# Optimization experiments

Hardware: AMD Instinct MI355X
Metric: run time of the kernel (lower is better)

Reference implementation:

```python
import jax, jax.numpy as jnp
import numpy as np

B, NK = 32, 1024
NUM_SAMPLES = 512
IT_MATCHES = 4
IT_RANSAC = 8
NUM_CORR = 5
INLIER_3D_TH = 0.15
INLIER_REF_TH = 0.15
NUM_REF_STEPS = 4
SCORE_TEMP = 10.0
TH_OUTLIERS = 0.35
MAX_LOSS_NULL = 0.5
SOFT_CLIP_M = 0.5
BETA = 5.0 / INLIER_3D_TH


def _gumbel(key, shape):
    u = jax.random.uniform(key, shape, minval=1e-6, maxval=1.0 - 1e-6)
    return -jnp.log(-jnp.log(u))


def _backproject(cor, d, K):
    # cor [B,S,2], d [B,S,2] (channel 0 is depth), K [B,3,3] -> [B,S,3]
    depth = d[..., :1]
    pts = jnp.concatenate([cor, jnp.ones_like(cor[..., :1])], -1)
    Kinv = jnp.linalg.inv(K)
    rays = jnp.einsum('bij,bsj->bsi', Kinv, pts)
    return depth * rays


def _procrustes(X, Y, w):
    # weighted Kabsch: find R,t with Y ~ R X + t. X,Y [B,N,3], w [B,N]
    wn = w / (jnp.sum(w, -1, keepdims=True) + 1e-8)
    muX = jnp.einsum('bn,bni->bi', wn, X)
    muY = jnp.einsum('bn,bni->bi', wn, Y)
    Xc = X - muX[:, None]
    Yc = Y - muY[:, None]
    H = jnp.einsum('bn,bni,bnj->bij', wn, Xc, Yc)  # [B,3,3]
    U, S, Vt = jnp.linalg.svd(H, full_matrices=False)
    V = jnp.swapaxes(Vt, -1, -2)
    Ut = jnp.swapaxes(U, -1, -2)
    d = jnp.linalg.det(V @ Ut)
    Vm = V * jnp.stack([jnp.ones_like(d), jnp.ones_like(d), d], -1)[:, None, :]
    R = Vm @ Ut
    t = muY - jnp.einsum('bij,bj->bi', R, muX)
    return R, t[:, None, :]


def _dist(X, Y, R, t):
    return jnp.linalg.norm(jnp.einsum('bij,bnj->bni', R, X) + t - Y, axis=-1)


def _pose_loss(R, t, Rgt, tgt):
    cosang = jnp.clip((jnp.einsum('bij,bij->b', R, Rgt) - 1.0) / 2.0, -0.999999, 0.999999)
    ang = jnp.arccos(cosang)
    terr = jnp.linalg.norm(t - tgt, axis=-1)[:, 0]
    sc = lambda x: SOFT_CLIP_M * jnp.tanh(x / SOFT_CLIP_M)
    lr = sc(ang)[:, None]
    lt = sc(terr)[:, None]
    return 0.5 * (lr + lt), lr, lt


def _rodrigues(axis, ang):
    x, y, z = axis[:, 0], axis[:, 1], axis[:, 2]
    zero = jnp.zeros_like(x)
    Kx = jnp.stack([zero, -z, y, z, zero, -x, -y, x, zero], -1).reshape(-1, 3, 3)
    I = jnp.eye(3, dtype=axis.dtype)[None]
    return I + jnp.sin(ang)[:, None, None] * Kx + (1.0 - jnp.cos(ang))[:, None, None] * (Kx @ Kx)


def setup_inputs():
    ks = jax.random.split(jax.random.key(0), 10)
    matches = jax.random.uniform(ks[0], (B, NK, NK), jnp.float32, 1e-4, 1.0)
    kps0 = jax.random.uniform(ks[1], (B, 2, NK), jnp.float32, 0.0, 640.0)
    kps1 = jax.random.uniform(ks[2], (B, 2, NK), jnp.float32, 0.0, 640.0)
    depth0 = jax.random.uniform(ks[3], (B, 2, NK), jnp.float32, 0.1, 10.0)
    depth1 = jax.random.uniform(ks[4], (B, 2, NK), jnp.float32, 0.1, 10.0)
    Kc = jnp.tile(jnp.array([[600.0, 0.0, 320.0], [0.0, 600.0, 240.0], [0.0, 0.0, 1.0]], jnp.float32)[None], (B, 1, 1))
    axis = jax.random.normal(ks[5], (B, 3))
    axis = axis / (jnp.linalg.norm(axis, axis=-1, keepdims=True) + 1e-8)
    ang = jax.random.uniform(ks[6], (B,), minval=0.0, maxval=0.5)
    R = _rodrigues(axis, ang)
    tvec = 0.3 * jax.random.normal(ks[7], (B, 3))
    T = jnp.zeros((B, 4, 4), jnp.float32).at[:, :3, :3].set(R).at[:, :3, 3].set(tvec).at[:, 3, 3].set(1.0)
    return dict(matches=matches, kps0=kps0, depth0=depth0, kps1=kps1, depth1=depth1,
                K0=Kc, K1=Kc, Kori_color0=Kc, T_0to1=T)


def _forward(matches, kps0, depth0, kps1, depth1, K0, K1, T_0to1):
    Rgt = T_0to1[:, :3, :3]
    tgt = T_0to1[:, :3, 3][:, None, :]
    matches_row = matches.reshape(B, NK * NK)
    logm = jnp.log(matches_row + 1e-12)
    bidx = jnp.arange(B)[:, None]
    kps0t = jnp.swapaxes(kps0, 1, 2)  # [B,NK,2]
    kps1t = jnp.swapaxes(kps1, 1, 2)
    d0t = jnp.swapaxes(depth0, 1, 2)
    d1t = jnp.swapaxes(depth1, 1, 2)
    key = jax.random.key(42)
    total = jnp.zeros((B, 1), jnp.float32)
    for _i in range(IT_MATCHES):
        key, km = jax.random.split(key)
        # multinomial-without-replacement via Gumbel top-k over the full match matrix
        _, sidx = jax.lax.top_k(logm + _gumbel(km, logm.shape), NUM_SAMPLES)  # [B,S]
        i0 = sidx // NK
        i1 = sidx % NK
        cor0 = kps0t[bidx, i0]
        cor1 = kps1t[bidx, i1]
        dd0 = d0t[bidx, i0]
        dd1 = d1t[bidx, i1]
        w = matches_row[bidx, sidx]  # sampling weights for RANSAC minimal sets
        X = _backproject(cor0, dd0, K0)
        Y = _backproject(cor1, dd1, K1)
        logw = jnp.log(w + 1e-12)
        scores, lvals = [], []
        for _kk in range(IT_RANSAC):
            key, kr = jax.random.split(key)
            _, ridx = jax.lax.top_k(logw + _gumbel(kr, logw.shape), NUM_CORR)  # [B,C]
            Xk = X[bidx, ridx]
            Yk = Y[bidx, ridx]
            R_pre, t_pre = _procrustes(Xk, Yk, jnp.ones((B, NUM_CORR), X.dtype))  # use_weights=False
            score_k = jnp.sum(jax.nn.sigmoid(BETA * (INLIER_3D_TH - _dist(X, Y, R_pre, t_pre))), -1, keepdims=True)
            # inlier refinement (no_grad in original)
            Xd = jax.lax.stop_gradient(X)
            Yd = jax.lax.stop_gradient(Y)
            Rd = jax.lax.stop_gradient(R_pre)
            td = jax.lax.stop_gradient(t_pre)
            inl_ref = jnp.zeros((B, NUM_SAMPLES), X.dtype).at[bidx, ridx].set(1.0)
            inl_pre = jnp.zeros((B,), X.dtype)
            for _r in range(NUM_REF_STEPS):
                inl = (_dist(Xd, Yd, Rd, td) < INLIER_REF_TH).astype(X.dtype)
                cnt = inl.sum(-1)
                do = (cnt >= NUM_CORR) & (cnt > inl_pre)
                inl_pre = cnt
                inl_ref = jnp.where(do[:, None], inl, inl_ref)
                Rn, tn = _procrustes(Xd, Yd, inl_ref)
                Rd = jnp.where(do[:, None, None], Rn, Rd)
                td = jnp.where(do[:, None, None], tn, td)
            R, t = _procrustes(X, Y, inl_ref)  # differentiable final fit
            lv, _lr, _lt = _pose_loss(R, t, Rgt, tgt)
            scores.append(score_k)
            lvals.append(lv)
        scores_r = jnp.concatenate(scores, -1)  # [B,IT_RANSAC]
        lvals_r = jnp.concatenate(lvals, -1)
        null_score = TH_OUTLIERS * NUM_SAMPLES * jnp.ones((B, 1), jnp.float32)
        null_loss = MAX_LOSS_NULL * jnp.ones((B, 1), jnp.float32)
        scores_n = jnp.concatenate([scores_r, null_score], -1)
        lvals_n = jnp.concatenate([lvals_r, null_loss], -1)
        sm = jax.nn.softmax(scores_n / SCORE_TEMP, -1)
        total = total + jnp.sum(lvals_n * sm, -1, keepdims=True)
    return total / IT_MATCHES


def reference(matches, kps0, depth0, kps1, depth1, K0, K1, Kori_color0, T_0to1):
    return _forward(matches, kps0, depth0, kps1, depth1, K0, K1, T_0to1)
```

## Files before the change

### kernel.cpp

```cpp
#include <hip/hip_runtime.h>
#include <stdint.h>

typedef unsigned long long u64;
typedef uint32_t u32;

#define NB 32
#define NKP 1024
#define ROWN (NKP*NKP)
#define NSAMP 512
#define ITM 4
#define ITR 8
#define NBIN 2048
#define KBASE 0xC0000000u
#define CHUNKS 64
#define SLOTS 256
#define QCAP 768

struct Keys { u32 km[ITM][2]; u32 kr[ITM][ITR][2]; };

__host__ __device__ static inline u32 rotl32(u32 x, int d) { return __builtin_rotateleft32(x, (unsigned)d); }

__host__ __device__ static inline void tf2x32(u32 k0, u32 k1, u32 x0, u32 x1, u32& o0, u32& o1)
{
    u32 ks2 = k0 ^ k1 ^ 0x1BD11BDAu;
    x0 += k0; x1 += k1;
#define TFR(r) { x0 += x1; x1 = rotl32(x1, r); x1 ^= x0; }
    TFR(13) TFR(15) TFR(26) TFR(6)
    x0 += k1; x1 += ks2 + 1u;
    TFR(17) TFR(29) TFR(16) TFR(24)
    x0 += ks2; x1 += k0 + 2u;
    TFR(13) TFR(15) TFR(26) TFR(6)
    x0 += k0; x1 += k1 + 3u;
    TFR(17) TFR(29) TFR(16) TFR(24)
    x0 += k1; x1 += ks2 + 4u;
    TFR(13) TFR(15) TFR(26) TFR(6)
    x0 += ks2; x1 += k0 + 5u;
#undef TFR
    o0 = x0; o1 = x1;
}

#define G_MINV 1e-6f
#define G_MAXV ((float)(1.0 - 1e-6))
#define G_SPAN (G_MAXV - G_MINV)

__device__ static inline float u_from_bits(u32 bits) {
    float f = __uint_as_float((bits >> 9) | 0x3f800000u) - 1.0f;
    float u = __fadd_rn(__fmul_rn(f, G_SPAN), G_MINV);
    return fmaxf(G_MINV, u);
}

#define EARLY_TH9 (8220000u << 9)

__device__ static inline u32 fkey(float v) {
    u32 u = __float_as_uint(v);
    return (u & 0x80000000u) ? ~u : (u | 0x80000000u);
}

__device__ static inline float wred(float v) {
    #pragma unroll
    for (int o = 1; o < 64; o <<= 1) v += __shfl_xor(v, o, 64);
    return v;
}

__device__ static inline u64 shfl_xor_u64(u64 v, int mask) {
    u32 lo = (u32)v, hi = (u32)(v >> 32);
    lo = __shfl_xor(lo, mask, 64);
    hi = __shfl_xor(hi, mask, 64);
    return ((u64)hi << 32) | (u64)lo;
}

__device__ static void kabsch(const float Hf[9], float Rf[9])
{
    double H00=Hf[0],H01=Hf[1],H02=Hf[2];
    double H10=Hf[3],H11=Hf[4],H12=Hf[5];
    double H20=Hf[6],H21=Hf[7],H22=Hf[8];
    double A00 = H00*H00 + H10*H10 + H20*H20;
    double A01 = H00*H01 + H10*H11 + H20*H21;
    double A02 = H00*H02 + H10*H12 + H20*H22;
    double A11 = H01*H01 + H11*H11 + H21*H21;
    double A12 = H01*H02 + H11*H12 + H21*H22;
    double A22 = H02*H02 + H12*H12 + H22*H22;
    double V00=1,V10=0,V20=0;
    double V01=0,V11=1,V21=0;
    double V02=0,V12=0,V22=1;
#define JROT(App,Aqq,Apq,Apr,Aqr, Vp0,Vp1,Vp2, Vq0,Vq1,Vq2) \
    if (fabs(Apq) > 0.0) { \
        double th = (Aqq - App) / (2.0 * Apq); \
        double tt = copysign(1.0, th) / (fabs(th) + sqrt(1.0 + th*th)); \
        double cc = 1.0 / sqrt(1.0 + tt*tt); \
        double ss = tt * cc; \
        double npp = App - tt*Apq, nqq = Aqq + tt*Apq; \
        double npr = cc*Apr - ss*Aqr, nqr = ss*Apr + cc*Aqr; \
        App = npp; Aqq = nqq; Apq = 0.0; Apr = npr; Aqr = nqr; \
        double tv; \
        tv = cc*Vp0 - ss*Vq0; Vq0 = ss*Vp0 + cc*Vq0; Vp0 = tv; \
        tv = cc*Vp1 - ss*Vq1; Vq1 = ss*Vp1 + cc*Vq1; Vp1 = tv; \
        tv = cc*Vp2 - ss*Vq2; Vq2 = ss*Vp2 + cc*Vq2; Vp2 = tv; \
    }
    for (int sw = 0; sw < 10; ++sw) {
        JROT(A00,A11,A01, A02,A12, V00,V10,V20, V01,V11,V21);
        JROT(A00,A22,A02, A01,A12, V00,V10,V20, V02,V12,V22);
        JROT(A11,A22,A12, A01,A02, V01,V11,V21, V02,V12,V22);
    }
#undef JROT
    double l0=A00, l1=A11, l2=A22;
    double e0[3]={V00,V10,V20}, e1[3]={V01,V11,V21}, e2[3]={V02,V12,V22};
    if (l0 < l1) { double t=l0;l0=l1;l1=t; for(int c=0;c<3;++c){double s=e0[c];e0[c]=e1[c];e1[c]=s;} }
    if (l0 < l2) { double t=l0;l0=l2;l2=t; for(int c=0;c<3;++c){double s=e0[c];e0[c]=e2[c];e2[c]=s;} }
    if (l1 < l2) { double t=l1;l1=l2;l2=t; for(int c=0;c<3;++c){double s=e1[c];e1[c]=e2[c];e2[c]=s;} }
    double u0[3], u1[3], u2[3];
#define HMUL(e,u) { u[0]=H00*e[0]+H01*e[1]+H02*e[2]; u[1]=H10*e[0]+H11*e[1]+H12*e[2]; u[2]=H20*e[0]+H21*e[1]+H22*e[2]; }
    HMUL(e0,u0) HMUL(e1,u1) HMUL(e2,u2)
#undef HMUL
    double s0 = sqrt(u0[0]*u0[0]+u0[1]*u0[1]+u0[2]*u0[2]);
    double s1 = sqrt(u1[0]*u1[0]+u1[1]*u1[1]+u1[2]*u1[2]);
    double s2 = sqrt(u2[0]*u2[0]+u2[1]*u2[1]+u2[2]*u2[2]);
    double eps = 1e-12 + 1e-6 * s0;
    if (s0 > 0.0) { u0[0]/=s0; u0[1]/=s0; u0[2]/=s0; } else { u0[0]=1.0; u0[1]=0.0; u0[2]=0.0; }
    if (s1 > eps) { u1[0]/=s1; u1[1]/=s1; u1[2]/=s1; }
    else {
        double ax0 = (fabs(u0[0]) < 0.9) ? 1.0 : 0.0;
        double ax1 = 1.0 - ax0;
        double dd = ax0*u0[0] + ax1*u0[1];
        double w0 = ax0 - dd*u0[0], w1 = ax1 - dd*u0[1], w2 = -dd*u0[2];
        double nn = sqrt(w0*w0+w1*w1+w2*w2);
        u1[0]=w0/nn; u1[1]=w1/nn; u1[2]=w2/nn;
    }
    if (s2 > eps) { u2[0]/=s2; u2[1]/=s2; u2[2]/=s2; }
    else {
        u2[0] = u0[1]*u1[2] - u0[2]*u1[1];
        u2[1] = u0[2]*u1[0] - u0[0]*u1[2];
        u2[2] = u0[0]*u1[1] - u0[1]*u1[0];
    }
    double M[3][3];
    #pragma unroll
    for (int i2=0;i2<3;++i2)
      #pragma unroll
      for (int j2=0;j2<3;++j2)
        M[i2][j2] = e0[i2]*u0[j2] + e1[i2]*u1[j2] + e2[i2]*u2[j2];
    double det = M[0][0]*(M[1][1]*M[2][2]-M[1][2]*M[2][1])
               - M[0][1]*(M[1][0]*M[2][2]-M[1][2]*M[2][0])
               + M[0][2]*(M[1][0]*M[2][1]-M[1][1]*M[2][0]);
    #pragma unroll
    for (int i2=0;i2<3;++i2)
      #pragma unroll
      for (int j2=0;j2<3;++j2)
        Rf[i2*3+j2] = (float)(e0[i2]*u0[j2] + e1[i2]*u1[j2] + det*(e2[i2]*u2[j2]));
}

__device__ static inline float dist1(const float R[9], const float t[3], const float x[3], const float y[3])
{
    float a = R[0]*x[0]+R[1]*x[1]+R[2]*x[2]+t[0]-y[0];
    float b = R[3]*x[0]+R[4]*x[1]+R[5]*x[2]+t[1]-y[1];
    float c = R[6]*x[0]+R[7]*x[1]+R[8]*x[2]+t[2]-y[2];
    return sqrtf(a*a+b*b+c*c);
}

__device__ static void proc512(const float (&X)[8][3], const float (&Y)[8][3], const float (&w)[8],
                               float R[9], float t[3])
{
    float sw = 0.f;
    #pragma unroll
    for (int q=0;q<8;++q) sw += w[q];
    float S = wred(sw) + 1e-8f;
    float wn[8];
    #pragma unroll
    for (int q=0;q<8;++q) wn[q] = w[q] / S;
    float mx[3], my[3];
    #pragma unroll
    for (int c=0;c<3;++c) {
        float ax=0.f, ay=0.f;
        #pragma unroll
        for (int q=0;q<8;++q) { ax += wn[q]*X[q][c]; ay += wn[q]*Y[q][c]; }
        mx[c] = wred(ax); my[c] = wred(ay);
    }
    float Hf[9];
    #pragma unroll
    for (int ci=0;ci<3;++ci)
      #pragma unroll
      for (int cj=0;cj<3;++cj) {
        float h=0.f;
        #pragma unroll
        for (int q=0;q<8;++q) h += wn[q]*(X[q][ci]-mx[ci])*(Y[q][cj]-my[cj]);
        Hf[ci*3+cj] = wred(h);
      }
    kabsch(Hf, R);
    #pragma unroll
    for (int c=0;c<3;++c) t[c] = my[c] - (R[c*3+0]*mx[0] + R[c*3+1]*mx[1] + R[c*3+2]*mx[2]);
}

__device__ static void inv3(const float* __restrict__ Kin, float* __restrict__ out)
{
    float a[3][6];
    for (int r=0;r<3;++r) for (int c=0;c<3;++c) { a[r][c]=Kin[r*3+c]; a[r][c+3] = (r==c)?1.f:0.f; }
    for (int col=0; col<3; ++col) {
        int piv = col;
        for (int r=col+1;r<3;++r) if (fabsf(a[r][col]) > fabsf(a[piv][col])) piv = r;
        if (piv != col) for (int c=0;c<6;++c) { float tt=a[col][c]; a[col][c]=a[piv][c]; a[piv][c]=tt; }
        float pv = a[col][col];
        for (int c=0;c<6;++c) a[col][c] /= pv;
        for (int r=0;r<3;++r) if (r != col) {
            float f = a[r][col];
            if (f != 0.f) for (int c=0;c<6;++c) a[r][c] -= f * a[col][c];
        }
    }
    for (int r=0;r<3;++r) for (int c=0;c<3;++c) out[r*3+c] = a[r][c+3];
}

static const size_t OFF_CNTS = 0;
static const size_t OFF_SC   = OFF_CNTS + (size_t)ITM*NB*CHUNKS*4;
static const size_t OFF_LV   = OFF_SC   + (size_t)ITM*NB*ITR*4;
static const size_t OFF_SAMP = OFF_LV   + (size_t)ITM*NB*ITR*4;
static const size_t OFF_CAND = OFF_SAMP + (size_t)ITM*NB*NSAMP*8*4;

__global__ __launch_bounds__(256) void kA(const float* __restrict__ mat, Keys keys,
                                          u64* __restrict__ candC, u32* __restrict__ cnts)
{
    __shared__ u64 lists[ITM][SLOTS];
    __shared__ u32 lcnt[ITM];
    __shared__ u32 qbits[QCAP];
    __shared__ float qm[QCAP];
    __shared__ u32 qji[QCAP];
    __shared__ u32 qcnt;
    int tid = threadIdx.x;
    int b = blockIdx.y;
    int chunk = blockIdx.x;
    if (tid < ITM) lcnt[tid] = 0;
    if (tid == 0) qcnt = 0;
    __syncthreads();
    const float4* rowp = reinterpret_cast<const float4*>(mat + (size_t)b * ROWN);
    int base = chunk * 4096;
    for (int itc = 0; itc < 16; ++itc) {
        int f4 = base + itc*256 + tid;
        float4 m4 = rowp[f4];
        float mv[4] = {m4.x, m4.y, m4.z, m4.w};
        u32 j0 = (u32)f4 * 4u;
        #pragma unroll
        for (int e = 0; e < 4; ++e) {
            u32 j = j0 + (u32)e;
            u32 flat = ((u32)b << 20) | j;
            #pragma unroll
            for (int i = 0; i < ITM; ++i) {
                u32 o0, o1; tf2x32(keys.km[i][0], keys.km[i][1], 0u, flat, o0, o1);
                u32 bits = o0 ^ o1;
                if (bits >= EARLY_TH9) {
                    u32 p = atomicAdd(&qcnt, 1u);
                    if (p < (u32)QCAP) {
                        qbits[p] = bits;
                        qm[p]    = mv[e];
                        qji[p]   = ((u32)i << 20) | j;
                    }
                }
            }
        }
        __syncthreads();
        u32 qn = qcnt; if (qn > (u32)QCAP) qn = QCAP;
        for (u32 t = tid; t < qn; t += 256) {
            u32 bits = qbits[t];
            float m  = qm[t];
            u32 ji   = qji[t];
            float u  = u_from_bits(bits);
            float g  = -logf(-logf(u));
            float lg = logf(m + 1e-12f);
            float v  = lg + g;
            if (v > 4.0f) {
                u32 i2 = ji >> 20;
                u32 jj = ji & 0xFFFFFu;
                u32 p = atomicAdd(&lcnt[i2], 1u);
                if (p < (u32)SLOTS)
                    lists[i2][p] = ((u64)fkey(v) << 32) | (u64)(u32)(~jj);
            }
        }
        __syncthreads();
        if (tid == 0) qcnt = 0;
        __syncthreads();
    }
    #pragma unroll
    for (int i = 0; i < ITM; ++i) {
        u32 n = lcnt[i]; if (n > (u32)SLOTS) n = SLOTS;
        for (u32 s = tid; s < n; s += 256)
            candC[(((size_t)(i*NB + b))*CHUNKS + chunk)*SLOTS + s] = lists[i][s];
    }
    if (tid < ITM) cnts[((size_t)(tid*NB + b))*CHUNKS + chunk] = min(lcnt[tid], (u32)SLOTS);
}

__global__ __launch_bounds__(256) void kD(const float* __restrict__ mat,
        const float* __restrict__ kps0, const float* __restrict__ dep0,
        const float* __restrict__ kps1, const float* __restrict__ dep1,
        const float* __restrict__ K0, const float* __restrict__ K1,
        const u64* __restrict__ candC, const u32* __restrict__ cnts,
        float* __restrict__ samp)
{
    int ib = blockIdx.x;
    int b = ib % NB;
    int tid = threadIdx.x;
    __shared__ u32 hist[NBIN];
    __shared__ u64 buf[2048];
    __shared__ u32 ccnt[CHUNKS];
    __shared__ u32 gs[64];
    __shared__ u32 nkeep, cutkey_s;
    __shared__ float Ki[2][9];
    for (int idx = tid; idx < NBIN; idx += 256) hist[idx] = 0;
    for (int idx = tid; idx < 2048; idx += 256) buf[idx] = 0ull;
    if (tid < CHUNKS) ccnt[tid] = cnts[(size_t)ib*CHUNKS + tid];
    if (tid == 0) nkeep = 0;
    __syncthreads();
    const u64* cd = candC + (size_t)ib * CHUNKS * SLOTS;
    for (int t = tid; t < CHUNKS*SLOTS; t += 256) {
        int c = t >> 8, s = t & (SLOTS-1);
        if ((u32)s < ccnt[c]) {
            u32 key = (u32)(cd[t] >> 32);
            u32 bin = (key - KBASE) >> 14;
            if (bin > (u32)(NBIN-1)) bin = NBIN-1;
            atomicAdd(&hist[bin], 1u);
        }
    }
    __syncthreads();
    if (tid < 64) {
        u32 ssum = 0;
        int top = NBIN-1 - tid*32;
        for (int k = 0; k < 32; ++k) ssum += hist[top - k];
        gs[tid] = ssum;
    }
    __syncthreads();
    if (tid == 0) {
        u32 cum = 0; int cutbin = -1;
        for (int g = 0; g < 64; ++g) {
            if (cum + gs[g] >= (u32)NSAMP) {
                int t2 = NBIN-1 - g*32;
                for (int k = 0; k < 32; ++k) {
                    u32 c = hist[t2 - k];
                    if (cum + c >= (u32)NSAMP) { cutbin = t2 - k; break; }
                    cum += c;
                }
                break;
            }
            cum += gs[g];
        }
        cutkey_s = (cutbin >= 0) ? (KBASE + ((u32)cutbin << 14)) : 0u;
    }
    __syncthreads();
    u32 cutkey = cutkey_s;
    for (int t = tid; t < CHUNKS*SLOTS; t += 256) {
        int c = t >> 8, s = t & (SLOTS-1);
        if ((u32)s < ccnt[c]) {
            u64 cv = cd[t];
            if ((u32)(cv >> 32) >= cutkey) {
                u32 p = atomicAdd(&nkeep, 1u);
                if (p < 2048u) buf[p] = cv;
            }
        }
    }
    __syncthreads();
    for (int k = 2; k <= 2048; k <<= 1) {
        for (int j = k >> 1; j > 0; j >>= 1) {
            for (int i2 = tid; i2 < 2048; i2 += 256) {
                int ixj = i2 ^ j;
                if (ixj > i2) {
                    bool up = ((i2 & k) == 0);
                    u64 a = buf[i2], c2 = buf[ixj];
                    bool dosw = up ? (a > c2) : (a < c2);
                    if (dosw) { buf[i2] = c2; buf[ixj] = a; }
                }
            }
            __syncthreads();
        }
    }
    if (tid == 0) { inv3(K0 + (size_t)b*9, Ki[0]); inv3(K1 + (size_t)b*9, Ki[1]); }
    __syncthreads();
    for (int r = tid; r < NSAMP; r += 256) {
        u64 c = buf[2047 - r];
        u32 j = (~(u32)(c & 0xFFFFFFFFull)) & (u32)(ROWN - 1);
        int i0 = (int)(j >> 10);
        int i1 = (int)(j & 1023u);
        float uu0 = kps0[(size_t)b*2*NKP + i0];
        float vv0 = kps0[(size_t)b*2*NKP + NKP + i0];
        float dd0 = dep0[(size_t)b*2*NKP + i0];
        float uu1 = kps1[(size_t)b*2*NKP + i1];
        float vv1 = kps1[(size_t)b*2*NKP + NKP + i1];
        float dd1 = dep1[(size_t)b*2*NKP + i1];
        float r0 = Ki[0][0]*uu0 + Ki[0][1]*vv0 + Ki[0][2];
        float r1 = Ki[0][3]*uu0 + Ki[0][4]*vv0 + Ki[0][5];
        float r2 = Ki[0][6]*uu0 + Ki[0][7]*vv0 + Ki[0][8];
        float q0 = Ki[1][0]*uu1 + Ki[1][1]*vv1 + Ki[1][2];
        float q1 = Ki[1][3]*uu1 + Ki[1][4]*vv1 + Ki[1][5];
        float q2 = Ki[1][6]*uu1 + Ki[1][7]*vv1 + Ki[1][8];
        float w = mat[(size_t)b*ROWN + j];
        float* sp = samp + ((size_t)ib*NSAMP + r)*8;
        sp[0] = dd0*r0; sp[1] = dd0*r1; sp[2] = dd0*r2;
        sp[3] = dd1*q0; sp[4] = dd1*q1; sp[5] = dd1*q2;
        sp[6] = logf(w + 1e-12f);
        sp[7] = 0.f;
    }
}

__global__ __launch_bounds__(64) void kE(const float* __restrict__ samp, const float* __restrict__ Tmat,
                                         Keys keys, float* __restrict__ scoreArr, float* __restrict__ lvArr)
{
    int blk = blockIdx.x;
    int kk = blk & 7;
    int ib = blk >> 3;
    int i = ib / NB;
    int b = ib % NB;
    int lane = threadIdx.x;
    const float* s = samp + (size_t)ib * NSAMP * 8;
    float X[8][3], Y[8][3], lw[8];
    #pragma unroll
    for (int q = 0; q < 8; ++q) {
        const float4* p = reinterpret_cast<const float4*>(s + (size_t)(q*64 + lane)*8);
        float4 a0 = p[0], a1 = p[1];
        X[q][0]=a0.x; X[q][1]=a0.y; X[q][2]=a0.z;
        Y[q][0]=a0.w; Y[q][1]=a1.x; Y[q][2]=a1.y;
        lw[q]=a1.z;
    }
    u64 comp[8];
    #pragma unroll
    for (int q = 0; q < 8; ++q) {
        u32 j = (u32)(q*64 + lane);
        u32 o0,o1; tf2x32(keys.kr[i][kk][0], keys.kr[i][kk][1], 0u, (u32)(b*NSAMP) + j, o0,o1);
        float u = u_from_bits(o0^o1);
        float g = -logf(-logf(u));
        float v = lw[q] + g;
        comp[q] = ((u64)fkey(v) << 32) | (u64)(u32)(~j);
    }
    int ridx[5];
    #pragma unroll
    for (int r = 0; r < 5; ++r) {
        u64 m = comp[0];
        #pragma unroll
        for (int q=1;q<8;++q) if (comp[q] > m) m = comp[q];
        #pragma unroll
        for (int o=1;o<64;o<<=1) { u64 x = shfl_xor_u64(m,o); if (x > m) m = x; }
        ridx[r] = (int)((~(u32)(m & 0xFFFFFFFFull)) & (u32)(NSAMP-1));
        #pragma unroll
        for (int q=0;q<8;++q) if (comp[q] == m) comp[q] = 0ull;
    }
    float Xk[5][3], Yk[5][3];
    #pragma unroll
    for (int r=0;r<5;++r) {
        const float* p = s + (size_t)ridx[r]*8;
        Xk[r][0]=p[0]; Xk[r][1]=p[1]; Xk[r][2]=p[2];
        Yk[r][0]=p[3]; Yk[r][1]=p[4]; Yk[r][2]=p[5];
    }
    float S5 = 5.0f + 1e-8f;
    float wn5 = 1.0f / S5;
    float mx[3]={0,0,0}, my[3]={0,0,0};
    #pragma unroll
    for (int r=0;r<5;++r) {
        #pragma unroll
        for (int c=0;c<3;++c) { mx[c] += wn5*Xk[r][c]; my[c] += wn5*Yk[r][c]; }
    }
    float Hf[9] = {0,0,0,0,0,0,0,0,0};
    #pragma unroll
    for (int r=0;r<5;++r)
      #pragma unroll
      for (int ci=0;ci<3;++ci)
        #pragma unroll
        for (int cj=0;cj<3;++cj)
          Hf[ci*3+cj] += wn5*(Xk[r][ci]-mx[ci])*(Yk[r][cj]-my[cj]);
    float Rpre[9], tpre[3];
    kabsch(Hf, Rpre);
    #pragma unroll
    for (int c=0;c<3;++c) tpre[c] = my[c] - (Rpre[c*3+0]*mx[0] + Rpre[c*3+1]*mx[1] + Rpre[c*3+2]*mx[2]);
    const float BETAF = (float)(5.0/0.15);
    float partial = 0.f;
    #pragma unroll
    for (int q=0;q<8;++q) {
        float d = dist1(Rpre, tpre, X[q], Y[q]);
        float z = BETAF * (0.15f - d);
        partial += 1.0f / (1.0f + expf(-z));
    }
    float score = wred(partial);
    float inlref[8];
    #pragma unroll
    for (int q=0;q<8;++q) {
        int j = q*64 + lane;
        inlref[q] = (j==ridx[0] || j==ridx[1] || j==ridx[2] || j==ridx[3] || j==ridx[4]) ? 1.0f : 0.0f;
    }
    float Rd[9], td[3];
    #pragma unroll
    for (int c2=0;c2<9;++c2) Rd[c2]=Rpre[c2];
    td[0]=tpre[0]; td[1]=tpre[1]; td[2]=tpre[2];
    float inl_pre = 0.f;
    for (int step=0; step<4; ++step) {
        float inl[8]; float csum = 0.f;
        #pragma unroll
        for (int q=0;q<8;++q) {
            float d = dist1(Rd, td, X[q], Y[q]);
            inl[q] = (d < 0.15f) ? 1.0f : 0.0f;
            csum += inl[q];
        }
        float cnt = wred(csum);
        bool doit = (cnt >= 5.0f) && (cnt > inl_pre);
        inl_pre = cnt;
        if (doit) {
            #pragma unroll
            for (int q=0;q<8;++q) inlref[q] = inl[q];
            proc512(X, Y, inlref, Rd, td);
        }
    }
    float Rfin[9], tfin[3];
    proc512(X, Y, inlref, Rfin, tfin);
    const float* Tb = Tmat + (size_t)b*16;
    float tr = 0.f;
    #pragma unroll
    for (int ci=0;ci<3;++ci)
      #pragma unroll
      for (int cj=0;cj<3;++cj)
        tr += Rfin[ci*3+cj] * Tb[ci*4+cj];
    float cosang = (tr - 1.0f) * 0.5f;
    cosang = fminf(fmaxf(cosang, -0.999999f), 0.999999f);
    float ang = acosf(cosang);
    float d0 = tfin[0]-Tb[3], d1 = tfin[1]-Tb[7], d2 = tfin[2]-Tb[11];
    float terr = sqrtf(d0*d0 + d1*d1 + d2*d2);
    float lr = 0.5f * tanhf(ang / 0.5f);
    float lt = 0.5f * tanhf(terr / 0.5f);
    float lv = 0.5f * (lr + lt);
    if (lane == 0) { scoreArr[blk] = score; lvArr[blk] = lv; }
}

__global__ void kF(const float* __restrict__ scoreArr, const float* __restrict__ lvArr, float* __restrict__ out)
{
    int b = threadIdx.x;
    if (b >= NB) return;
    const float NULLSC = (float)(0.35 * 512.0);
    float total = 0.f;
    for (int i = 0; i < ITM; ++i) {
        float x[9], lvv[9], ee[9];
        for (int k = 0; k < 8; ++k) {
            x[k] = scoreArr[(i*NB + b)*ITR + k] / 10.0f;
            lvv[k] = lvArr[(i*NB + b)*ITR + k];
        }
        x[8] = NULLSC / 10.0f;
        lvv[8] = 0.5f;
        float m = x[0];
        for (int k = 1; k < 9; ++k) m = fmaxf(m, x[k]);
        float Ssum = 0.f;
        for (int k = 0; k < 9; ++k) { ee[k] = expf(x[k] - m); Ssum += ee[k]; }
        float acc = 0.f;
        for (int k = 0; k < 9; ++k) acc += lvv[k] * (ee[k] / Ssum);
        total += acc;
    }
    out[b] = total / 4.0f;
}

extern "C" void kernel_launch(void* const* d_in, const int* in_sizes, int n_in,
                              void* d_out, int out_size, void* d_ws, size_t ws_size,
                              hipStream_t stream)
{
    (void)in_sizes; (void)n_in; (void)out_size; (void)ws_size;
    const float* mat  = (const float*)d_in[0];
    const float* kps0 = (const float*)d_in[1];
    const float* dep0 = (const float*)d_in[2];
    const float* kps1 = (const float*)d_in[3];
    const float* dep1 = (const float*)d_in[4];
    const float* K0   = (const float*)d_in[5];
    const float* K1   = (const float*)d_in[6];
    const float* Tm   = (const float*)d_in[8];
    float* out = (float*)d_out;

    Keys keys;
    {
        u32 k0 = 0u, k1 = 42u;
        for (int i = 0; i < ITM; ++i) {
            u32 a0,a1,b0,b1;
            tf2x32(k0,k1, 0u,0u, a0,a1);
            tf2x32(k0,k1, 0u,1u, b0,b1);
            k0=a0; k1=a1; keys.km[i][0]=b0; keys.km[i][1]=b1;
            for (int kk = 0; kk < ITR; ++kk) {
                tf2x32(k0,k1, 0u,0u, a0,a1);
                tf2x32(k0,k1, 0u,1u, b0,b1);
                k0=a0; k1=a1; keys.kr[i][kk][0]=b0; keys.kr[i][kk][1]=b1;
            }
        }
    }
    char* ws = (char*)d_ws;
    u32* cnts       = (u32*)(ws + OFF_CNTS);
    float* scoreArr = (float*)(ws + OFF_SC);
    float* lvArr    = (float*)(ws + OFF_LV);
    float* samp     = (float*)(ws + OFF_SAMP);
    u64* candC      = (u64*)(ws + OFF_CAND);

    kA<<<dim3(CHUNKS, NB), 256, 0, stream>>>(mat, keys, candC, cnts);
    kD<<<ITM*NB, 256, 0, stream>>>(mat, kps0, dep0, kps1, dep1, K0, K1, candC, cnts, samp);
    kE<<<ITM*NB*ITR, 64, 0, stream>>>(samp, Tm, keys, scoreArr, lvArr);
    kF<<<1, 64, 0, stream>>>(scoreArr, lvArr, out);
}
```

Before: 406.8 us.

## Gather match values only for queued candidates instead of streaming full matrix

The candidate pass no longer streams every match value through float4 loads. It hashes indices only, packs bits, iteration and index into a single 64-bit shared queue entry, and loads the match value from global memory just for the queued candidates. Queue flushes drop from 16 to 4 per chunk, so there are fewer block barriers, and the queue capacity grows to fit the larger batches. The trade-off is scattered global gathers, and a higher risk of the queue overflowing and silently dropping candidates.

```diff
diff --git a/kernel.cpp b/kernel.cpp
--- a/kernel.cpp
+++ b/kernel.cpp
@@ -14,7 +14,7 @@
 #define KBASE 0xC0000000u
 #define CHUNKS 64
 #define SLOTS 256
-#define QCAP 768
+#define QCAP 1024
 
 struct Keys { u32 km[ITM][2]; u32 kr[ITM][ITR][2]; };
 
@@ -218,9 +218,7 @@
 {
     __shared__ u64 lists[ITM][SLOTS];
     __shared__ u32 lcnt[ITM];
-    __shared__ u32 qbits[QCAP];
-    __shared__ float qm[QCAP];
-    __shared__ u32 qji[QCAP];
+    __shared__ u64 q[QCAP];
     __shared__ u32 qcnt;
     int tid = threadIdx.x;
     int b = blockIdx.y;
@@ -228,16 +226,11 @@
     if (tid < ITM) lcnt[tid] = 0;
     if (tid == 0) qcnt = 0;
     __syncthreads();
-    const float4* rowp = reinterpret_cast<const float4*>(mat + (size_t)b * ROWN);
-    int base = chunk * 4096;
-    for (int itc = 0; itc < 16; ++itc) {
-        int f4 = base + itc*256 + tid;
-        float4 m4 = rowp[f4];
-        float mv[4] = {m4.x, m4.y, m4.z, m4.w};
-        u32 j0 = (u32)f4 * 4u;
-        #pragma unroll
-        for (int e = 0; e < 4; ++e) {
-            u32 j = j0 + (u32)e;
+    const float* rowb = mat + (size_t)b * ROWN;
+    u32 jbase = (u32)chunk * 16384u + (u32)tid;
+    for (int seg = 0; seg < 4; ++seg) {
+        for (int lp = 0; lp < 16; ++lp) {
+            u32 j = jbase + (u32)((seg*16 + lp) << 8);
             u32 flat = ((u32)b << 20) | j;
             #pragma unroll
             for (int i = 0; i < ITM; ++i) {
@@ -245,27 +238,23 @@
                 u32 bits = o0 ^ o1;
                 if (bits >= EARLY_TH9) {
                     u32 p = atomicAdd(&qcnt, 1u);
-                    if (p < (u32)QCAP) {
-                        qbits[p] = bits;
-                        qm[p]    = mv[e];
-                        qji[p]   = ((u32)i << 20) | j;
-                    }
+                    if (p < (u32)QCAP)
+                        q[p] = ((u64)bits << 32) | ((u64)(u32)i << 20) | (u64)j;
                 }
             }
         }
         __syncthreads();
         u32 qn = qcnt; if (qn > (u32)QCAP) qn = QCAP;
         for (u32 t = tid; t < qn; t += 256) {
-            u32 bits = qbits[t];
-            float m  = qm[t];
-            u32 ji   = qji[t];
+            u64 e  = q[t];
+            u32 bits = (u32)(e >> 32);
+            u32 i2 = ((u32)e >> 20) & 3u;
+            u32 jj = (u32)e & 0xFFFFFu;
+            float m  = rowb[jj];
             float u  = u_from_bits(bits);
             float g  = -logf(-logf(u));
-            float lg = logf(m + 1e-12f);
-            float v  = lg + g;
+            float v  = logf(m + 1e-12f) + g;
             if (v > 4.0f) {
-                u32 i2 = ji >> 20;
-                u32 jj = ji & 0xFFFFFu;
                 u32 p = atomicAdd(&lcnt[i2], 1u);
                 if (p < (u32)SLOTS)
                     lists[i2][p] = ((u64)fkey(v) << 32) | (u64)(u32)(~jj);
```

Measured after the change: 400.1 us. About the same (-1.6%).
